# Kernel optimization log

Measured on AMD Instinct MI355X. Metric: run time of the kernel, lower is better.

The kernel has to match this reference:

```python
import jax, jax.numpy as jnp
import numpy as np

B, LQ, DM, DFFN, NL, NH, NP = 4, 13294, 256, 1024, 4, 8, 4
HD = DM // NH
SHAPES = np.array([[100, 100], [50, 50], [25, 25], [13, 13]], dtype=np.int64)


def _ln(x, g, b):
    m = x.mean(-1, keepdims=True)
    v = ((x - m) ** 2).mean(-1, keepdims=True)
    return (x - m) / jnp.sqrt(v + 1e-5) * g + b


def _ms_deform(value, loc, aw, shapes):
    # value: [B, Lv, NH, HD]; loc: [B, Lq, NH, NL, NP, 2]; aw: [B, Lq, NH, NL, NP]
    Bn, Lq = loc.shape[0], loc.shape[1]
    offs = np.concatenate([[0], np.cumsum(shapes[:, 0] * shapes[:, 1])])
    out = jnp.zeros((Bn, NH, Lq, HD), value.dtype)
    for l in range(NL):
        H, W = int(shapes[l, 0]), int(shapes[l, 1])
        val = value[:, offs[l]:offs[l + 1]].transpose(0, 2, 1, 3)  # [B,NH,HW,HD]
        # grid_sample align_corners=False convention: pixel = norm*size - 0.5
        x = (loc[:, :, :, l, :, 0] * W - 0.5).transpose(0, 2, 1, 3).reshape(Bn, NH, Lq * NP)
        y = (loc[:, :, :, l, :, 1] * H - 0.5).transpose(0, 2, 1, 3).reshape(Bn, NH, Lq * NP)
        x0 = jnp.floor(x); y0 = jnp.floor(y)
        fx = x - x0; fy = y - y0
        acc = jnp.zeros((Bn, NH, Lq * NP, HD), value.dtype)
        for dy, dx in ((0, 0), (0, 1), (1, 0), (1, 1)):
            xi = x0 + dx; yi = y0 + dy
            w = (fx if dx else 1.0 - fx) * (fy if dy else 1.0 - fy)
            valid = (xi >= 0) & (xi < W) & (yi >= 0) & (yi < H)  # zero padding
            idx = (jnp.clip(yi, 0, H - 1) * W + jnp.clip(xi, 0, W - 1)).astype(jnp.int32)
            g = jnp.take_along_axis(val, idx[..., None], axis=2)  # [B,NH,Lq*NP,HD]
            acc = acc + g * (w * valid)[..., None]
        a = aw[:, :, :, l].transpose(0, 2, 1, 3).reshape(Bn, NH, Lq * NP)
        out = out + (acc * a[..., None]).reshape(Bn, NH, Lq, NP, HD).sum(3)
    return out.transpose(0, 2, 1, 3).reshape(Bn, Lq, NH * HD)


def _forward(src, pos, reference_points, shapes, Wv, bv, Ws, bs, Wa, ba, Wo, bo,
             W1, b1, W2, b2, g1, be1, g2, be2):
    Bn, Lq, _ = src.shape
    q = src + pos
    value = (src @ Wv + bv).reshape(Bn, Lq, NH, HD)
    off = (q @ Ws + bs).reshape(Bn, Lq, NH, NL, NP, 2)
    aw = jax.nn.softmax((q @ Wa + ba).reshape(Bn, Lq, NH, NL * NP), axis=-1)
    aw = aw.reshape(Bn, Lq, NH, NL, NP)
    norm = jnp.asarray(np.ascontiguousarray(shapes[:, ::-1]), jnp.float32)  # (W,H) per level
    loc = reference_points[:, :, None, :, None, :] + off / norm[None, None, None, :, None, :]
    attn = _ms_deform(value, loc, aw, shapes) @ Wo + bo
    x = _ln(src + attn, g1, be1)
    h = jax.nn.relu(x @ W1 + b1)
    return _ln(x + h @ W2 + b2, g2, be2)


def setup_inputs():
    key = jax.random.key(0)
    ks = jax.random.split(key, 12)

    def lin(k, i, o):
        k1, k2 = jax.random.split(k)
        return (0.02 * jax.random.normal(k1, (i, o), jnp.float32),
                0.02 * jax.random.normal(k2, (o,), jnp.float32))

    Wv, bv = lin(ks[0], DM, DM)
    Ws, bs = lin(ks[1], DM, NH * NL * NP * 2)
    Wa, ba = lin(ks[2], DM, NH * NL * NP)
    Wo, bo = lin(ks[3], DM, DM)
    W1, b1 = lin(ks[4], DM, DFFN)
    W2, b2 = lin(ks[5], DFFN, DM)
    lsi = np.concatenate([[0], np.cumsum(SHAPES[:, 0] * SHAPES[:, 1])[:-1]])
    return {
        "src": jax.random.normal(ks[6], (B, LQ, DM), jnp.float32),
        "pos": jax.random.normal(ks[7], (B, LQ, DM), jnp.float32),
        "reference_points": jax.random.uniform(ks[8], (B, LQ, NL, 2), jnp.float32),
        "spatial_shapes": jnp.asarray(SHAPES),
        "level_start_index": jnp.asarray(lsi),
        "Wv": Wv, "bv": bv, "Ws": Ws, "bs": bs, "Wa": Wa, "ba": ba,
        "Wo": Wo, "bo": bo, "W1": W1, "b1": b1, "W2": W2, "b2": b2,
        "g1": jnp.ones((DM,), jnp.float32), "be1": jnp.zeros((DM,), jnp.float32),
        "g2": jnp.ones((DM,), jnp.float32), "be2": jnp.zeros((DM,), jnp.float32),
    }


def reference(src, pos, reference_points, spatial_shapes, level_start_index,
              Wv, bv, Ws, bs, Wa, ba, Wo, bo, W1, b1, W2, b2, g1, be1, g2, be2):
    shapes = np.asarray(spatial_shapes)
    return _forward(src, pos, reference_points, shapes, Wv, bv, Ws, bs, Wa, ba,
                    Wo, bo, W1, b1, W2, b2, g1, be1, g2, be2)
```

## Files before the change

### kernel.cpp

```cpp
#include <hip/hip_runtime.h>


#define LQn   13294
#define MREAL 53176
#define MP    53248
#define MT    416
#define MHALF 26588
#define MTH   208

typedef __attribute__((ext_vector_type(8))) short short8;
typedef __attribute__((ext_vector_type(4))) short short4v;
typedef __attribute__((ext_vector_type(4))) float f32x4;
typedef __attribute__((ext_vector_type(2))) float f32x2;

__device__ __forceinline__ short f2bf(float f) {
    unsigned u = __float_as_uint(f);
    unsigned r = (u + 0x7FFFu + ((u >> 16) & 1u)) >> 16;
    return (short)r;
}
__device__ __forceinline__ float bf2f(short b) {
    return __uint_as_float(((unsigned)(unsigned short)b) << 16);
}
__device__ __forceinline__ f32x2 bf2x2(unsigned r) {
    f32x2 o;
    o.x = __uint_as_float(r << 16);
    o.y = __uint_as_float(r & 0xffff0000u);
    return o;
}

#define GLOAD16(gp, lp)                                                        \
    __builtin_amdgcn_global_load_lds(                                          \
        (const __attribute__((address_space(1))) void*)(gp),                   \
        (__attribute__((address_space(3))) void*)(lp), 16, 0, 0)

__global__ __launch_bounds__(256) void prep_all(
    const float* __restrict__ Wv, const float* __restrict__ Ws,
    const float* __restrict__ Wa, const float* __restrict__ Wo,
    const float* __restrict__ W1, const float* __restrict__ W2,
    const float* __restrict__ bs, const float* __restrict__ ba,
    const float* __restrict__ src, const float* __restrict__ pos,
    short* __restrict__ WvT, short* __restrict__ WsaT,
    short* __restrict__ WoT, short* __restrict__ W1T,
    short* __restrict__ W2T, float* __restrict__ bsa,
    short* __restrict__ q_bf, short* __restrict__ src_bf) {
    const int bid = blockIdx.x, tid = threadIdx.x;
    if (bid >= 2945) {
        const int i = (bid - 2945) * 256 + tid;
        if (i < MREAL * 32) {
            const float4 a0 = ((const float4*)src)[i * 2];
            const float4 a1 = ((const float4*)src)[i * 2 + 1];
            const float4 b0 = ((const float4*)pos)[i * 2];
            const float4 b1 = ((const float4*)pos)[i * 2 + 1];
            short8 o, o2;
            o[0] = f2bf(a0.x + b0.x); o[1] = f2bf(a0.y + b0.y);
            o[2] = f2bf(a0.z + b0.z); o[3] = f2bf(a0.w + b0.w);
            o[4] = f2bf(a1.x + b1.x); o[5] = f2bf(a1.y + b1.y);
            o[6] = f2bf(a1.z + b1.z); o[7] = f2bf(a1.w + b1.w);
            o2[0] = f2bf(a0.x); o2[1] = f2bf(a0.y);
            o2[2] = f2bf(a0.z); o2[3] = f2bf(a0.w);
            o2[4] = f2bf(a1.x); o2[5] = f2bf(a1.y);
            o2[6] = f2bf(a1.z); o2[7] = f2bf(a1.w);
            ((short8*)q_bf)[i] = o;
            ((short8*)src_bf)[i] = o2;
        }
        return;
    }
    const float* W; short* WT; int K, N, base;
    if (bid < 256)       { W = Wv; WT = WvT;              K = 256;  N = 256;  base = 0; }
    else if (bid < 512)  { W = Ws; WT = WsaT;             K = 256;  N = 256;  base = 256; }
    else if (bid < 640)  { W = Wa; WT = WsaT + 256 * 256; K = 256;  N = 128;  base = 512; }
    else if (bid < 896)  { W = Wo; WT = WoT;              K = 256;  N = 256;  base = 640; }
    else if (bid < 1920) { W = W1; WT = W1T;              K = 256;  N = 1024; base = 896; }
    else if (bid < 2944) { W = W2; WT = W2T;              K = 1024; N = 256;  base = 1920; }
    else {
        if (tid < 256) bsa[tid] = bs[tid];
        else if (tid < 384) bsa[tid] = ba[tid - 256];
        return;
    }
    const int i = (bid - base) * 256 + tid;
    const int n = i / K, k = i - n * K;
    WT[i] = f2bf(W[(size_t)k * N + n]);
}

template <int EPI, int NT>
__global__ __launch_bounds__(256) void gemm_bt(const short* __restrict__ Ab,
                                               const short* __restrict__ BT,
                                               const float* __restrict__ bias,
                                               void* C,
                                               int M, int K, int N,
                                               int ldb, int ldc) {
    const int d = blockIdx.x;
    const int c = d & 7, j = d >> 3;
    const int jg = j / NT;
    const int m0 = (c + 8 * jg) * 128;
    const int n0 = (j - jg * NT) * 128;
    const int t = threadIdx.x;
    const int wid = t >> 6, lane = t & 63;
    const int wr = wid >> 1, wc = wid & 1;
    const int quad = lane >> 4, l16 = lane & 15;

    __shared__ short lA[2][128 * 32];
    __shared__ short lB[2][128 * 32];

    f32x4 acc[4][4];
#pragma unroll
    for (int i = 0; i < 4; ++i)
#pragma unroll
        for (int jj = 0; jj < 4; ++jj) acc[i][jj] = (f32x4){0.f, 0.f, 0.f, 0.f};

    const int grow = wid * 32 + (lane >> 2);
    const int gcol = (lane & 3) * 8;
    auto stage = [&](int buf, int k0) {
        GLOAD16(Ab + (size_t)(m0 + grow) * K + k0 + gcol,
                &lA[buf][(wid * 32) * 32]);
        GLOAD16(Ab + (size_t)(m0 + grow + 16) * K + k0 + gcol,
                &lA[buf][(wid * 32 + 16) * 32]);
        GLOAD16(BT + (size_t)(n0 + grow) * ldb + k0 + gcol,
                &lB[buf][(wid * 32) * 32]);
        GLOAD16(BT + (size_t)(n0 + grow + 16) * ldb + k0 + gcol,
                &lB[buf][(wid * 32 + 16) * 32]);
    };
    stage(0, 0);
    __syncthreads();
    int cur = 0;
    for (int k0 = 0; k0 < K; k0 += 32) {
        if (k0 + 32 < K) stage(cur ^ 1, k0 + 32);
        short8 af[4], bfr[4];
#pragma unroll
        for (int mi = 0; mi < 4; ++mi)
            af[mi] = *(const short8*)&lA[cur][(wr * 64 + mi * 16 + l16) * 32 + quad * 8];
#pragma unroll
        for (int ni = 0; ni < 4; ++ni)
            bfr[ni] = *(const short8*)&lB[cur][(wc * 64 + ni * 16 + l16) * 32 + quad * 8];
#pragma unroll
        for (int mi = 0; mi < 4; ++mi)
#pragma unroll
            for (int ni = 0; ni < 4; ++ni)
                acc[mi][ni] = __builtin_amdgcn_mfma_f32_16x16x32_bf16(
                    af[mi], bfr[ni], acc[mi][ni], 0, 0, 0);
        __syncthreads();
        cur ^= 1;
    }

    short* lflat = (short*)lA;
#pragma unroll
    for (int p = 0; p < 2; ++p) {
        if (wc == p) {
#pragma unroll
            for (int ni = 0; ni < 4; ++ni) {
                const int lc = ni * 16 + l16;
                const float bia = bias[n0 + p * 64 + lc];
#pragma unroll
                for (int mi = 0; mi < 4; ++mi)
#pragma unroll
                    for (int r = 0; r < 4; ++r) {
                        const int lr = wr * 64 + mi * 16 + quad * 4 + r;
                        float v = acc[mi][ni][r] + bia;
                        if (EPI == 2) v = fmaxf(v, 0.f);
                        lflat[lr * 64 + (lc ^ ((lr & 7) << 3))] = f2bf(v);
                    }
            }
        }
        __syncthreads();
#pragma unroll
        for (int i = 0; i < 4; ++i) {
            const int chunk = i * 256 + t;
            const int row = chunk >> 3;
            const int c8 = (chunk & 7) * 8;
            const int gr = m0 + row;
            if (gr < M) {
                const short8 v8 =
                    *(const short8*)&lflat[row * 64 + (c8 ^ ((row & 7) << 3))];
                const int gcl = n0 + p * 64 + c8;
                if (EPI == 5) {
                    const int b = gr / LQn, s = gr - b * LQn;
                    const int hh = gcl >> 5, dd = gcl & 31;
                    *(short8*)&((short*)C)[(((size_t)b * 8 + hh) * LQn + s) * 32 + dd] = v8;
                } else {
                    *(short8*)&((short*)C)[(size_t)gr * ldc + gcl] = v8;
                }
            }
        }
        __syncthreads();
    }
}

template <int EPI>
__global__ __launch_bounds__(512) void gemm_ln(const short* __restrict__ Ab,
                                               const short* __restrict__ BT,
                                               const float* __restrict__ bias,
                                               const void* __restrict__ resid,
                                               void* __restrict__ out,
                                               const float* __restrict__ g,
                                               const float* __restrict__ be,
                                               int M, int K, int resbf) {
    const int t = threadIdx.x;
    const int m0 = blockIdx.x * 128;
    const int wid = t >> 6, lane = t & 63;
    const int wr = wid >> 2, wc = wid & 3;
    const int quad = lane >> 4, l16 = lane & 15;

    __shared__ short lA[2][128 * 32];
    __shared__ short lB[2][256 * 32];
    __shared__ float2 part[128][4];
    __shared__ float2 stats[128];

    f32x4 acc[4][4];
#pragma unroll
    for (int i = 0; i < 4; ++i)
#pragma unroll
        for (int j = 0; j < 4; ++j) acc[i][j] = (f32x4){0.f, 0.f, 0.f, 0.f};

    const int ga_row = wid * 16 + (lane >> 2);
    const int gb_row = wid * 32 + (lane >> 2);
    const int gcol8 = (lane & 3) * 8;
    auto stage = [&](int buf, int k0) {
        GLOAD16(Ab + (size_t)(m0 + ga_row) * K + k0 + gcol8,
                &lA[buf][(wid * 16) * 32]);
        GLOAD16(BT + (size_t)gb_row * K + k0 + gcol8,
                &lB[buf][(wid * 32) * 32]);
        GLOAD16(BT + (size_t)(gb_row + 16) * K + k0 + gcol8,
                &lB[buf][(wid * 32 + 16) * 32]);
    };
    stage(0, 0);
    __syncthreads();
    int cur = 0;
    for (int k0 = 0; k0 < K; k0 += 32) {
        if (k0 + 32 < K) stage(cur ^ 1, k0 + 32);
        short8 af[4], bfr[4];
#pragma unroll
        for (int mi = 0; mi < 4; ++mi)
            af[mi] = *(const short8*)&lA[cur][(wr * 64 + mi * 16 + l16) * 32 + quad * 8];
#pragma unroll
        for (int ni = 0; ni < 4; ++ni)
            bfr[ni] = *(const short8*)&lB[cur][(wc * 64 + ni * 16 + l16) * 32 + quad * 8];
#pragma unroll
        for (int mi = 0; mi < 4; ++mi)
#pragma unroll
            for (int ni = 0; ni < 4; ++ni)
                acc[mi][ni] = __builtin_amdgcn_mfma_f32_16x16x32_bf16(
                    af[mi], bfr[ni], acc[mi][ni], 0, 0, 0);
        __syncthreads();
        cur ^= 1;
    }

    float biasv[4], gv[4], bev[4];
    int gcs[4];
#pragma unroll
    for (int ni = 0; ni < 4; ++ni) {
        gcs[ni] = wc * 64 + ni * 16 + l16;
        biasv[ni] = bias[gcs[ni]];
        gv[ni] = g[gcs[ni]];
        bev[ni] = be[gcs[ni]];
    }
#pragma unroll
    for (int mi = 0; mi < 4; ++mi) {
#pragma unroll
        for (int r = 0; r < 4; ++r) {
            const int lr = wr * 64 + mi * 16 + quad * 4 + r;
            const int gr = m0 + lr;
            const bool ok = (gr < M);
            float s1 = 0.f, s2 = 0.f;
#pragma unroll
            for (int ni = 0; ni < 4; ++ni) {
                float v = acc[mi][ni][r] + biasv[ni];
                if (ok) {
                    if (resbf)
                        v += bf2f(((const short*)resid)[(size_t)gr * 256 + gcs[ni]]);
                    else
                        v += ((const float*)resid)[(size_t)gr * 256 + gcs[ni]];
                }
                acc[mi][ni][r] = v;
                s1 += v;
                s2 += v * v;
            }
#pragma unroll
            for (int o = 1; o < 16; o <<= 1) {
                s1 += __shfl_xor(s1, o);
                s2 += __shfl_xor(s2, o);
            }
            if (l16 == 0) part[lr][wc] = make_float2(s1, s2);
        }
    }
    __syncthreads();
    if (t < 128) {
        float s1 = 0.f, s2 = 0.f;
#pragma unroll
        for (int w = 0; w < 4; ++w) {
            const float2 p = part[t][w];
            s1 += p.x;
            s2 += p.y;
        }
        const float mean = s1 * (1.0f / 256.0f);
        const float var = s2 * (1.0f / 256.0f) - mean * mean;
        stats[t] = make_float2(mean, rsqrtf(var + 1e-5f));
    }
    __syncthreads();

    if (EPI == 0) {
        short* lflat = (short*)lA;
#pragma unroll
        for (int p = 0; p < 4; ++p) {
            if (wc == p) {
#pragma unroll
                for (int mi = 0; mi < 4; ++mi)
#pragma unroll
                    for (int r = 0; r < 4; ++r) {
                        const int lr = wr * 64 + mi * 16 + quad * 4 + r;
                        const float2 st = stats[lr];
#pragma unroll
                        for (int ni = 0; ni < 4; ++ni) {
                            const int lc = ni * 16 + l16;
                            const float v =
                                (acc[mi][ni][r] - st.x) * st.y * gv[ni] + bev[ni];
                            lflat[lr * 64 + (lc ^ ((lr & 7) << 3))] = f2bf(v);
                        }
                    }
            }
            __syncthreads();
#pragma unroll
            for (int i = 0; i < 2; ++i) {
                const int chunk = i * 512 + t;
                const int row = chunk >> 3;
                const int c8 = (chunk & 7) * 8;
                const int gr = m0 + row;
                if (gr < M) {
                    const short8 v8 =
                        *(const short8*)&lflat[row * 64 + (c8 ^ ((row & 7) << 3))];
                    *(short8*)&((short*)out)[(size_t)gr * 256 + p * 64 + c8] = v8;
                }
            }
            __syncthreads();
        }
    } else {
#pragma unroll
        for (int mi = 0; mi < 4; ++mi) {
#pragma unroll
            for (int r = 0; r < 4; ++r) {
                const int lr = wr * 64 + mi * 16 + quad * 4 + r;
                const int gr = m0 + lr;
                if (gr < M) {
                    const float2 st = stats[lr];
#pragma unroll
                    for (int ni = 0; ni < 4; ++ni) {
                        const float v =
                            (acc[mi][ni][r] - st.x) * st.y * gv[ni] + bev[ni];
                        ((float*)out)[(size_t)gr * 256 + gcs[ni]] = v;
                    }
                }
            }
        }
    }
}

__global__ __launch_bounds__(256) void sample_k(const short* __restrict__ value,
                                                const short* __restrict__ offaw,
                                                const float* __restrict__ refp,
                                                short* __restrict__ attn,
                                                int nwg) {
    int wg = blockIdx.x;
    {
        const int q = nwg >> 3, r = nwg & 7;
        const int xcd = wg & 7, idx = wg >> 3;
        wg = (xcd < r ? xcd * (q + 1) : r * (q + 1) + (xcd - r) * q) + idx;
    }
    const int tid = threadIdx.x;
    const int grp = wg * 16 + (tid >> 4);
    const int s16 = tid & 15;
    const int l = s16 >> 2, sub = s16 & 3;
    const int row = grp >> 3, h = grp & 7;
    const int b = row / LQn;
    const int L = (l == 0) ? 100 : (l == 1) ? 50 : (l == 2) ? 25 : 13;
    const int O = (l == 0) ? 0 : (l == 1) ? 10000 : (l == 2) ? 12500 : 13125;
    const float Lf = (float)L;

    const short* op = offaw + (size_t)row * 384 + h * 32;
    const short* ap = offaw + (size_t)row * 384 + 256 + h * 16;

    const short4v alog = *(const short4v*)(ap + l * 4);
    float lg[4];
#pragma unroll
    for (int j = 0; j < 4; ++j) lg[j] = bf2f(alog[j]);
    float m = fmaxf(fmaxf(lg[0], lg[1]), fmaxf(lg[2], lg[3]));
    m = fmaxf(m, __shfl_xor(m, 4));
    m = fmaxf(m, __shfl_xor(m, 8));
    float s = 0.f;
#pragma unroll
    for (int j = 0; j < 4; ++j) { lg[j] = __expf(lg[j] - m); s += lg[j]; }
    s += __shfl_xor(s, 4);
    s += __shfl_xor(s, 8);
    const float inv = 1.f / s;

    const float2 rxy = *(const float2*)(refp + (size_t)row * 8 + l * 2);
    const short8 ov = *(const short8*)(op + l * 8);
    const short* vlev = value + ((size_t)(b * 8 + h) * LQn + O) * 32 + sub * 8;

    f32x2 acc2[4];
#pragma unroll
    for (int j = 0; j < 4; ++j) acc2[j] = (f32x2){0.f, 0.f};

#pragma unroll 2
    for (int p = 0; p < 4; ++p) {
        const float x = fmaf(rxy.x, Lf, bf2f(ov[p * 2 + 0]) - 0.5f);
        const float y = fmaf(rxy.y, Lf, bf2f(ov[p * 2 + 1]) - 0.5f);
        const float xf = floorf(x), yf = floorf(y);
        const int ix = (int)xf, iy = (int)yf;
        const float fx = x - xf, fy = y - yf;
        const float aw = lg[p] * inv;
        const float vx0 = ((unsigned)ix < (unsigned)L) ? 1.f : 0.f;
        const float vx1 = ((unsigned)(ix + 1) < (unsigned)L) ? 1.f : 0.f;
        const float vy0 = ((unsigned)iy < (unsigned)L) ? 1.f : 0.f;
        const float vy1 = ((unsigned)(iy + 1) < (unsigned)L) ? 1.f : 0.f;
        const float gx0 = (1.f - fx) * aw, gx1 = fx * aw;
        const float w00 = gx0 * (1.f - fy) * vx0 * vy0;
        const float w10 = gx1 * (1.f - fy) * vx1 * vy0;
        const float w01 = gx0 * fy * vx0 * vy1;
        const float w11 = gx1 * fy * vx1 * vy1;
        const int ix0 = min(max(ix, 0), L - 1);
        const int ix1 = min(max(ix + 1, 0), L - 1);
        const int iy0 = min(max(iy, 0), L - 1);
        const int iy1 = min(max(iy + 1, 0), L - 1);
        const int ro0 = iy0 * L, ro1 = iy1 * L;
        const uint4 c00 = *(const uint4*)(vlev + ((ro0 + ix0) << 5));
        const uint4 c10 = *(const uint4*)(vlev + ((ro0 + ix1) << 5));
        const uint4 c01 = *(const uint4*)(vlev + ((ro1 + ix0) << 5));
        const uint4 c11 = *(const uint4*)(vlev + ((ro1 + ix1) << 5));
        const unsigned* p00 = (const unsigned*)&c00;
        const unsigned* p10 = (const unsigned*)&c10;
        const unsigned* p01 = (const unsigned*)&c01;
        const unsigned* p11 = (const unsigned*)&c11;
#pragma unroll
        for (int j = 0; j < 4; ++j)
            acc2[j] += w00 * bf2x2(p00[j]) + w10 * bf2x2(p10[j]) +
                       w01 * bf2x2(p01[j]) + w11 * bf2x2(p11[j]);
    }

    float acc[8];
#pragma unroll
    for (int j = 0; j < 4; ++j) {
        acc[j * 2] = acc2[j].x;
        acc[j * 2 + 1] = acc2[j].y;
    }
#pragma unroll
    for (int j = 0; j < 8; ++j) {
        acc[j] += __shfl_xor(acc[j], 4);
        acc[j] += __shfl_xor(acc[j], 8);
    }

    if (l == 0) {
        short8 o;
#pragma unroll
        for (int j = 0; j < 8; ++j) o[j] = f2bf(acc[j]);
        *(short8*)(attn + (size_t)row * 256 + h * 32 + sub * 8) = o;
    }
}

extern "C" void kernel_launch(void* const* d_in, const int* in_sizes, int n_in,
                              void* d_out, int out_size, void* d_ws, size_t ws_size,
                              hipStream_t stream) {
    (void)in_sizes; (void)n_in; (void)out_size;
    const float* src  = (const float*)d_in[0];
    const float* pos  = (const float*)d_in[1];
    const float* refp = (const float*)d_in[2];
    const float* Wv = (const float*)d_in[5];
    const float* bv = (const float*)d_in[6];
    const float* Ws = (const float*)d_in[7];
    const float* bs = (const float*)d_in[8];
    const float* Wa = (const float*)d_in[9];
    const float* ba = (const float*)d_in[10];
    const float* Wo = (const float*)d_in[11];
    const float* bo = (const float*)d_in[12];
    const float* W1 = (const float*)d_in[13];
    const float* b1 = (const float*)d_in[14];
    const float* W2 = (const float*)d_in[15];
    const float* b2 = (const float*)d_in[16];
    const float* g1 = (const float*)d_in[17];
    const float* be1 = (const float*)d_in[18];
    const float* g2 = (const float*)d_in[19];
    const float* be2 = (const float*)d_in[20];

    char* ws = (char*)d_ws;
    size_t off = 0;
    auto take = [&](size_t bytes) {
        char* p = ws + off;
        off += (bytes + 255) & ~(size_t)255;
        return p;
    };
    short* WvT  = (short*)take(256 * 256 * 2);
    short* WsaT = (short*)take(384 * 256 * 2);
    short* WoT  = (short*)take(256 * 256 * 2);
    short* W1T  = (short*)take(1024 * 256 * 2);
    short* W2T  = (short*)take(256 * 1024 * 2);
    float* bsa  = (float*)take(384 * 4);
    short* value_h = (short*)take((size_t)MP * 256 * 2);
    short* offaw   = (short*)take((size_t)MP * 384 * 2);
    short* attn_bf = (short*)take((size_t)MP * 256 * 2);

    short* src_bf;
    int resbf_g4;
    if (off + (size_t)MP * 256 * 2 <= ws_size) {
        src_bf = (short*)take((size_t)MP * 256 * 2);
        resbf_g4 = 1;
    } else {
        src_bf = offaw;
        resbf_g4 = 0;
    }

    short* q_bf = attn_bf;
    short* x_bf = value_h;
    short* h    = offaw;
    float* z    = (float*)d_out;

    prep_all<<<9593, 256, 0, stream>>>(Wv, Ws, Wa, Wo, W1, W2, bs, ba, src, pos,
                                       WvT, WsaT, WoT, W1T, W2T, bsa, q_bf,
                                       src_bf);
    gemm_bt<5, 2><<<832, 256, 0, stream>>>(
        src_bf, WvT, bv, value_h, MREAL, 256, 256, 256, 256);
    gemm_bt<1, 3><<<1248, 256, 0, stream>>>(
        q_bf, WsaT, bsa, offaw, MREAL, 256, 384, 256, 384);
    {
        const int nwg = (MREAL * 8) / 16;
        sample_k<<<nwg, 256, 0, stream>>>(value_h, offaw, refp, attn_bf, nwg);
    }
    gemm_ln<0><<<MT, 512, 0, stream>>>(attn_bf, WoT, bo,
                                       resbf_g4 ? (const void*)src_bf
                                                : (const void*)src,
                                       x_bf, g1, be1, MREAL, 256, resbf_g4);
    for (int half = 0; half < 2; ++half) {
        const size_t ro = (size_t)half * MHALF;
        gemm_bt<2, 8><<<1664, 256, 0, stream>>>(
            x_bf + ro * 256, W1T, b1, h, MHALF, 256, 1024, 256, 1024);
        gemm_ln<1><<<MTH, 512, 0, stream>>>(h, W2T, b2, x_bf + ro * 256,
                                            z + ro * 256, g2, be2, MHALF, 1024,
                                            1);
    }
}
```

Before: 415.7 us.

## Merge value/offset GEMMs, halve LN-GEMM row tiles, run FFN unsplit when workspace allows

Merges the value-projection and offset/attention-weight GEMMs into one launch by dispatching on block index. The fused GEMM+LayerNorm kernels move to 64-row tiles, which doubles the grid to improve occupancy across CUs. When the workspace is large enough, the FFN runs as one full-size pass over all rows instead of two halves, relying on the h buffer overlapping the earlier buffers. This cuts launches and tail effects. The cost is more redundant loading of B tiles per row in the LN kernels and a more intricate workspace aliasing scheme.

```diff
diff --git a/kernel.cpp b/kernel.cpp
--- a/kernel.cpp
+++ b/kernel.cpp
@@ -4,9 +4,7 @@
 #define LQn   13294
 #define MREAL 53176
 #define MP    53248
-#define MT    416
 #define MHALF 26588
-#define MTH   208
 
 typedef __attribute__((ext_vector_type(8))) short short8;
 typedef __attribute__((ext_vector_type(4))) short short4v;
@@ -83,13 +81,13 @@
 }
 
 template <int EPI, int NT>
-__global__ __launch_bounds__(256) void gemm_bt(const short* __restrict__ Ab,
-                                               const short* __restrict__ BT,
-                                               const float* __restrict__ bias,
-                                               void* C,
-                                               int M, int K, int N,
-                                               int ldb, int ldc) {
-    const int d = blockIdx.x;
+__device__ __forceinline__ void gemm_body(short* lA, short* lB,
+                                          const short* __restrict__ Ab,
+                                          const short* __restrict__ BT,
+                                          const float* __restrict__ bias,
+                                          void* C, int d,
+                                          int M, int K, int N,
+                                          int ldb, int ldc) {
     const int c = d & 7, j = d >> 3;
     const int jg = j / NT;
     const int m0 = (c + 8 * jg) * 128;
@@ -99,9 +97,6 @@
     const int wr = wid >> 1, wc = wid & 1;
     const int quad = lane >> 4, l16 = lane & 15;
 
-    __shared__ short lA[2][128 * 32];
-    __shared__ short lB[2][128 * 32];
-
     f32x4 acc[4][4];
 #pragma unroll
     for (int i = 0; i < 4; ++i)
@@ -112,13 +107,13 @@
     const int gcol = (lane & 3) * 8;
     auto stage = [&](int buf, int k0) {
         GLOAD16(Ab + (size_t)(m0 + grow) * K + k0 + gcol,
-                &lA[buf][(wid * 32) * 32]);
+                &lA[buf * 4096 + (wid * 32) * 32]);
         GLOAD16(Ab + (size_t)(m0 + grow + 16) * K + k0 + gcol,
-                &lA[buf][(wid * 32 + 16) * 32]);
+                &lA[buf * 4096 + (wid * 32 + 16) * 32]);
         GLOAD16(BT + (size_t)(n0 + grow) * ldb + k0 + gcol,
-                &lB[buf][(wid * 32) * 32]);
+                &lB[buf * 4096 + (wid * 32) * 32]);
         GLOAD16(BT + (size_t)(n0 + grow + 16) * ldb + k0 + gcol,
-                &lB[buf][(wid * 32 + 16) * 32]);
+                &lB[buf * 4096 + (wid * 32 + 16) * 32]);
     };
     stage(0, 0);
     __syncthreads();
@@ -128,10 +123,10 @@
         short8 af[4], bfr[4];
 #pragma unroll
         for (int mi = 0; mi < 4; ++mi)
-            af[mi] = *(const short8*)&lA[cur][(wr * 64 + mi * 16 + l16) * 32 + quad * 8];
+            af[mi] = *(const short8*)&lA[cur * 4096 + (wr * 64 + mi * 16 + l16) * 32 + quad * 8];
 #pragma unroll
         for (int ni = 0; ni < 4; ++ni)
-            bfr[ni] = *(const short8*)&lB[cur][(wc * 64 + ni * 16 + l16) * 32 + quad * 8];
+            bfr[ni] = *(const short8*)&lB[cur * 4096 + (wc * 64 + ni * 16 + l16) * 32 + quad * 8];
 #pragma unroll
         for (int mi = 0; mi < 4; ++mi)
 #pragma unroll
@@ -142,7 +137,7 @@
         cur ^= 1;
     }
 
-    short* lflat = (short*)lA;
+    short* lflat = lA;
 #pragma unroll
     for (int p = 0; p < 2; ++p) {
         if (wc == p) {
@@ -185,6 +180,35 @@
     }
 }
 
+template <int EPI, int NT>
+__global__ __launch_bounds__(256) void gemm_bt(const short* __restrict__ Ab,
+                                               const short* __restrict__ BT,
+                                               const float* __restrict__ bias,
+                                               void* C, int M, int K, int N,
+                                               int ldb, int ldc) {
+    __shared__ short sA[2 * 128 * 32];
+    __shared__ short sB[2 * 128 * 32];
+    gemm_body<EPI, NT>(sA, sB, Ab, BT, bias, C, blockIdx.x, M, K, N, ldb, ldc);
+}
+
+__global__ __launch_bounds__(256) void gemm12(const short* __restrict__ src_bf,
+                                              const short* __restrict__ WvT,
+                                              const float* __restrict__ bv,
+                                              short* __restrict__ value_h,
+                                              const short* __restrict__ q_bf,
+                                              const short* __restrict__ WsaT,
+                                              const float* __restrict__ bsa,
+                                              short* __restrict__ offaw) {
+    __shared__ short sA[2 * 128 * 32];
+    __shared__ short sB[2 * 128 * 32];
+    if (blockIdx.x < 832)
+        gemm_body<5, 2>(sA, sB, src_bf, WvT, bv, value_h, blockIdx.x,
+                        MREAL, 256, 256, 256, 256);
+    else
+        gemm_body<1, 3>(sA, sB, q_bf, WsaT, bsa, offaw, blockIdx.x - 832,
+                        MREAL, 256, 384, 256, 384);
+}
+
 template <int EPI>
 __global__ __launch_bounds__(512) void gemm_ln(const short* __restrict__ Ab,
                                                const short* __restrict__ BT,
@@ -195,28 +219,28 @@
                                                const float* __restrict__ be,
                                                int M, int K, int resbf) {
     const int t = threadIdx.x;
-    const int m0 = blockIdx.x * 128;
+    const int m0 = blockIdx.x * 64;
     const int wid = t >> 6, lane = t & 63;
     const int wr = wid >> 2, wc = wid & 3;
     const int quad = lane >> 4, l16 = lane & 15;
 
-    __shared__ short lA[2][128 * 32];
+    __shared__ short lA[2][64 * 32];
     __shared__ short lB[2][256 * 32];
-    __shared__ float2 part[128][4];
-    __shared__ float2 stats[128];
-
-    f32x4 acc[4][4];
-#pragma unroll
-    for (int i = 0; i < 4; ++i)
+    __shared__ float2 part[64][4];
+    __shared__ float2 stats[64];
+
+    f32x4 acc[2][4];
+#pragma unroll
+    for (int i = 0; i < 2; ++i)
 #pragma unroll
         for (int j = 0; j < 4; ++j) acc[i][j] = (f32x4){0.f, 0.f, 0.f, 0.f};
 
-    const int ga_row = wid * 16 + (lane >> 2);
     const int gb_row = wid * 32 + (lane >> 2);
     const int gcol8 = (lane & 3) * 8;
     auto stage = [&](int buf, int k0) {
-        GLOAD16(Ab + (size_t)(m0 + ga_row) * K + k0 + gcol8,
-                &lA[buf][(wid * 16) * 32]);
+        if (wid < 4)
+            GLOAD16(Ab + (size_t)(m0 + wid * 16 + (lane >> 2)) * K + k0 + gcol8,
+                    &lA[buf][(wid * 16) * 32]);
         GLOAD16(BT + (size_t)gb_row * K + k0 + gcol8,
                 &lB[buf][(wid * 32) * 32]);
         GLOAD16(BT + (size_t)(gb_row + 16) * K + k0 + gcol8,
@@ -227,15 +251,15 @@
     int cur = 0;
     for (int k0 = 0; k0 < K; k0 += 32) {
         if (k0 + 32 < K) stage(cur ^ 1, k0 + 32);
-        short8 af[4], bfr[4];
-#pragma unroll
-        for (int mi = 0; mi < 4; ++mi)
-            af[mi] = *(const short8*)&lA[cur][(wr * 64 + mi * 16 + l16) * 32 + quad * 8];
+        short8 af[2], bfr[4];
+#pragma unroll
+        for (int mi = 0; mi < 2; ++mi)
+            af[mi] = *(const short8*)&lA[cur][(wr * 32 + mi * 16 + l16) * 32 + quad * 8];
 #pragma unroll
         for (int ni = 0; ni < 4; ++ni)
             bfr[ni] = *(const short8*)&lB[cur][(wc * 64 + ni * 16 + l16) * 32 + quad * 8];
 #pragma unroll
-        for (int mi = 0; mi < 4; ++mi)
+        for (int mi = 0; mi < 2; ++mi)
 #pragma unroll
             for (int ni = 0; ni < 4; ++ni)
                 acc[mi][ni] = __builtin_amdgcn_mfma_f32_16x16x32_bf16(
@@ -254,10 +278,10 @@
         bev[ni] = be[gcs[ni]];
     }
 #pragma unroll
-    for (int mi = 0; mi < 4; ++mi) {
+    for (int mi = 0; mi < 2; ++mi) {
 #pragma unroll
         for (int r = 0; r < 4; ++r) {
-            const int lr = wr * 64 + mi * 16 + quad * 4 + r;
+            const int lr = wr * 32 + mi * 16 + quad * 4 + r;
             const int gr = m0 + lr;
             const bool ok = (gr < M);
             float s1 = 0.f, s2 = 0.f;
@@ -283,7 +307,7 @@
         }
     }
     __syncthreads();
-    if (t < 128) {
+    if (t < 64) {
         float s1 = 0.f, s2 = 0.f;
 #pragma unroll
         for (int w = 0; w < 4; ++w) {
@@ -303,10 +327,10 @@
         for (int p = 0; p < 4; ++p) {
             if (wc == p) {
 #pragma unroll
-                for (int mi = 0; mi < 4; ++mi)
+                for (int mi = 0; mi < 2; ++mi)
 #pragma unroll
                     for (int r = 0; r < 4; ++r) {
-                        const int lr = wr * 64 + mi * 16 + quad * 4 + r;
+                        const int lr = wr * 32 + mi * 16 + quad * 4 + r;
                         const float2 st = stats[lr];
 #pragma unroll
                         for (int ni = 0; ni < 4; ++ni) {
@@ -318,11 +342,9 @@
                     }
             }
             __syncthreads();
-#pragma unroll
-            for (int i = 0; i < 2; ++i) {
-                const int chunk = i * 512 + t;
-                const int row = chunk >> 3;
-                const int c8 = (chunk & 7) * 8;
+            {
+                const int row = t >> 3;
+                const int c8 = (t & 7) * 8;
                 const int gr = m0 + row;
                 if (gr < M) {
                     const short8 v8 =
@@ -334,10 +356,10 @@
         }
     } else {
 #pragma unroll
-        for (int mi = 0; mi < 4; ++mi) {
+        for (int mi = 0; mi < 2; ++mi) {
 #pragma unroll
             for (int r = 0; r < 4; ++r) {
-                const int lr = wr * 64 + mi * 16 + quad * 4 + r;
+                const int lr = wr * 32 + mi * 16 + quad * 4 + r;
                 const int gr = m0 + lr;
                 if (gr < M) {
                     const float2 st = stats[lr];
@@ -492,14 +514,27 @@
     short* W1T  = (short*)take(1024 * 256 * 2);
     short* W2T  = (short*)take(256 * 1024 * 2);
     float* bsa  = (float*)take(384 * 4);
-    short* value_h = (short*)take((size_t)MP * 256 * 2);
-    short* offaw   = (short*)take((size_t)MP * 384 * 2);
-    short* attn_bf = (short*)take((size_t)MP * 256 * 2);
-
+
+    const size_t SZ_VH = (size_t)MP * 256 * 2;
+    const size_t SZ_OF = (size_t)MP * 384 * 2;
+    const size_t SZ_H  = (size_t)MP * 1024 * 2;
+    const size_t SZ_HX = SZ_H - (SZ_OF + 2 * SZ_VH);
+
+    short* value_h = (short*)take(SZ_VH);
+    short* offaw   = (short*)take(SZ_OF);
+    short* attn_bf = (short*)take(SZ_VH);
+
+    const size_t rem = (off <= ws_size) ? ws_size - off : 0;
+    const bool cfgFull = rem >= SZ_VH + SZ_HX + 512;
+    const bool cfgA    = !cfgFull && rem >= SZ_VH + 256;
     short* src_bf;
     int resbf_g4;
-    if (off + (size_t)MP * 256 * 2 <= ws_size) {
-        src_bf = (short*)take((size_t)MP * 256 * 2);
+    if (cfgFull) {
+        src_bf = (short*)take(SZ_VH);
+        (void)take(SZ_HX);
+        resbf_g4 = 1;
+    } else if (cfgA) {
+        src_bf = (short*)take(SZ_VH);
         resbf_g4 = 1;
     } else {
         src_bf = offaw;
@@ -514,24 +549,29 @@
     prep_all<<<9593, 256, 0, stream>>>(Wv, Ws, Wa, Wo, W1, W2, bs, ba, src, pos,
                                        WvT, WsaT, WoT, W1T, W2T, bsa, q_bf,
                                        src_bf);
-    gemm_bt<5, 2><<<832, 256, 0, stream>>>(
-        src_bf, WvT, bv, value_h, MREAL, 256, 256, 256, 256);
-    gemm_bt<1, 3><<<1248, 256, 0, stream>>>(
-        q_bf, WsaT, bsa, offaw, MREAL, 256, 384, 256, 384);
+    gemm12<<<2080, 256, 0, stream>>>(src_bf, WvT, bv, value_h,
+                                     q_bf, WsaT, bsa, offaw);
     {
         const int nwg = (MREAL * 8) / 16;
         sample_k<<<nwg, 256, 0, stream>>>(value_h, offaw, refp, attn_bf, nwg);
     }
-    gemm_ln<0><<<MT, 512, 0, stream>>>(attn_bf, WoT, bo,
-                                       resbf_g4 ? (const void*)src_bf
-                                                : (const void*)src,
-                                       x_bf, g1, be1, MREAL, 256, resbf_g4);
-    for (int half = 0; half < 2; ++half) {
-        const size_t ro = (size_t)half * MHALF;
-        gemm_bt<2, 8><<<1664, 256, 0, stream>>>(
-            x_bf + ro * 256, W1T, b1, h, MHALF, 256, 1024, 256, 1024);
-        gemm_ln<1><<<MTH, 512, 0, stream>>>(h, W2T, b2, x_bf + ro * 256,
-                                            z + ro * 256, g2, be2, MHALF, 1024,
-                                            1);
-    }
-}
+    gemm_ln<0><<<MP / 64, 512, 0, stream>>>(attn_bf, WoT, bo,
+                                            resbf_g4 ? (const void*)src_bf
+                                                     : (const void*)src,
+                                            x_bf, g1, be1, MREAL, 256, resbf_g4);
+    if (cfgFull) {
+        gemm_bt<2, 8><<<3328, 256, 0, stream>>>(
+            x_bf, W1T, b1, h, MREAL, 256, 1024, 256, 1024);
+        gemm_ln<1><<<MP / 64, 512, 0, stream>>>(h, W2T, b2, x_bf, z, g2, be2,
+                                                MREAL, 1024, 1);
+    } else {
+        for (int half = 0; half < 2; ++half) {
+            const size_t ro = (size_t)half * MHALF;
+            gemm_bt<2, 8><<<1664, 256, 0, stream>>>(
+                x_bf + ro * 256, W1T, b1, h, MHALF, 256, 1024, 256, 1024);
+            gemm_ln<1><<<(MHALF + 63) / 64, 512, 0, stream>>>(
+                h, W2T, b2, x_bf + ro * 256, z + ro * 256, g2, be2, MHALF, 1024,
+                1);
+        }
+    }
+}
```

New measurement: 366.4 us. 1.13x faster.
